# Kernel optimization log

Hardware: AMD Instinct MI355X
Metric: run time of the kernel (lower is better)

The kernel has to match this reference:

```python
import jax, jax.numpy as jnp
import numpy as np

N = 100000
E = 1600000
D_PCA = 50
D_BIO = 64
HID = 32
HEADS = 4
OUT = 50
EPS = 1e-5


def setup_inputs() -> dict:
    key = jax.random.key(0)
    ks = jax.random.split(key, 32)
    g = lambda i, shape, s=0.05: jax.random.normal(ks[i], shape, dtype=jnp.float32) * s
    inp = {
        'x_pca': jax.random.normal(ks[0], (N, D_PCA), dtype=jnp.float32),
        'x_bio': jax.random.normal(ks[1], (N, D_BIO), dtype=jnp.float32),
        'edge_index': jax.random.randint(ks[2], (2, E), 0, N, dtype=jnp.int32),
        # bio encoder: Linear(64,16) -> BN(16) -> ELU -> Linear(16,16) -> ELU
        'bioW1': g(3, (16, D_BIO)), 'biob1': g(4, (16,)),
        'bn0_g': 1.0 + g(5, (16,)), 'bn0_b': g(6, (16,)),
        'bn0_m': g(7, (16,)), 'bn0_v': 1.0 + 0.1 * jax.random.uniform(ks[8], (16,), dtype=jnp.float32),
        'bioW2': g(9, (16, 16)), 'biob2': g(10, (16,)),
        # GATv2 layer 1: in = 50+16 = 66, out = HEADS*HID concat
        'Wl1': g(11, (HEADS * HID, D_PCA + 16)), 'bl1': g(12, (HEADS * HID,)),
        'Wr1': g(13, (HEADS * HID, D_PCA + 16)), 'br1': g(14, (HEADS * HID,)),
        'att1': g(15, (HEADS, HID)), 'bias1': g(16, (HEADS * HID,)),
        'bn1_g': 1.0 + g(17, (HEADS * HID,)), 'bn1_b': g(18, (HEADS * HID,)),
        'bn1_m': g(19, (HEADS * HID,)), 'bn1_v': 1.0 + 0.1 * jax.random.uniform(ks[20], (HEADS * HID,), dtype=jnp.float32),
        # GATv2 layer 2: in = HEADS*HID, heads=1, concat=False
        'Wl2': g(21, (HID, HEADS * HID)), 'bl2': g(22, (HID,)),
        'Wr2': g(23, (HID, HEADS * HID)), 'br2': g(24, (HID,)),
        'att2': g(25, (1, HID)), 'bias2': g(26, (HID,)),
        'bn2_g': 1.0 + g(27, (HID,)), 'bn2_b': g(28, (HID,)),
        'bn2_m': g(29, (HID,)), 'bn2_v': 1.0 + 0.1 * jax.random.uniform(ks[30], (HID,), dtype=jnp.float32),
        'predW': g(31, (OUT, HID)), 'predb': jnp.zeros((OUT,), dtype=jnp.float32),
    }
    return inp


def _bn(h, gm, bt, mean, var):
    # BatchNorm1d in eval mode (running stats)
    return (h - mean) * jax.lax.rsqrt(var + EPS) * gm + bt


def _gatv2(x, src, dst, Wl, bl, Wr, br, att, bias, heads, out_dim, concat):
    n = x.shape[0]
    xl = (x @ Wl.T + bl).reshape(n, heads, out_dim)  # source transform
    xr = (x @ Wr.T + br).reshape(n, heads, out_dim)  # target transform
    e = jax.nn.leaky_relu(xl[src] + xr[dst], 0.2)    # [E,H,C]
    logits = jnp.einsum('ehc,hc->eh', e, att)        # [E,H]
    m = jax.ops.segment_max(logits, dst, num_segments=n)
    a = jnp.exp(logits - m[dst])
    denom = jax.ops.segment_sum(a, dst, num_segments=n)
    alpha = a / (denom[dst] + 1e-16)                 # segment softmax over dst
    out = jax.ops.segment_sum(xl[src] * alpha[..., None], dst, num_segments=n)
    out = out.reshape(n, heads * out_dim) if concat else out.mean(axis=1)
    return out + bias


def reference(x_pca, x_bio, edge_index,
              bioW1, biob1, bn0_g, bn0_b, bn0_m, bn0_v, bioW2, biob2,
              Wl1, bl1, Wr1, br1, att1, bias1, bn1_g, bn1_b, bn1_m, bn1_v,
              Wl2, bl2, Wr2, br2, att2, bias2, bn2_g, bn2_b, bn2_m, bn2_v,
              predW, predb):
    n = x_pca.shape[0]
    # add self-loops (PyG GATv2Conv default)
    loop = jnp.arange(n, dtype=edge_index.dtype)
    src = jnp.concatenate([edge_index[0], loop])
    dst = jnp.concatenate([edge_index[1], loop])

    # bio encoder
    h_bio = jax.nn.elu(_bn(x_bio @ bioW1.T + biob1, bn0_g, bn0_b, bn0_m, bn0_v))
    h_bio = jax.nn.elu(h_bio @ bioW2.T + biob2)
    x = jnp.concatenate([x_pca, h_bio], axis=1)  # [N, 66]

    h = _gatv2(x, src, dst, Wl1, bl1, Wr1, br1, att1, bias1, HEADS, HID, True)
    h = jax.nn.elu(_bn(h, bn1_g, bn1_b, bn1_m, bn1_v))  # dropout off (eval)
    h = _gatv2(h, src, dst, Wl2, bl2, Wr2, br2, att2, bias2, 1, HID, False)
    h = jax.nn.elu(_bn(h, bn2_g, bn2_b, bn2_m, bn2_v))
    return h @ predW.T + predb
```

## Files before the change

kernel.cpp:

```cpp
#include <hip/hip_runtime.h>
#include <hip/hip_fp16.h>
#include <cstdint>
#include <cstddef>

#define NN 100000
#define NE 1600000
#define NEP (NE + NN)
#define NBLK 200
#define CHUNK ((NEP + NBLK - 1) / NBLK)
#define NBUCK2 ((NN + 255) / 256)
#define HISTN (NBUCK2 * NBLK)
#define HSCAN_BLOCKS ((HISTN + 1023) / 1024)

typedef __attribute__((ext_vector_type(8))) _Float16 half8;
typedef __attribute__((ext_vector_type(4))) float float4v;

__device__ __forceinline__ float elu_f(float x) {
    return x > 0.f ? x : __expf(x) - 1.f;
}

template<int N>
__device__ __forceinline__ float rrot_add(float x) {
    int s = __builtin_amdgcn_update_dpp(0, __float_as_int(x), 0x120 | N, 0xF, 0xF, true);
    return x + __int_as_float(s);
}
__device__ __forceinline__ float row16_allsum(float x) {
    x = rrot_add<1>(x); x = rrot_add<2>(x); x = rrot_add<4>(x); x = rrot_add<8>(x);
    return x;
}


__global__ __launch_bounds__(256) void part_hist(const int* __restrict__ ei, int* __restrict__ hist)
{
    __shared__ int cnt[NBUCK2];
    int tid = threadIdx.x, k = blockIdx.x;
    for (int i = tid; i < NBUCK2; i += 256) cnt[i] = 0;
    __syncthreads();
    int e0 = k * CHUNK, e1 = min(e0 + CHUNK, NEP);
    for (int e = e0 + tid; e < e1; e += 256) {
        int dst = (e < NE) ? ei[NE + e] : e - NE;
        atomicAdd(&cnt[dst >> 8], 1);
    }
    __syncthreads();
    for (int i = tid; i < NBUCK2; i += 256) hist[i * NBLK + k] = cnt[i];
}

__global__ __launch_bounds__(256) void scan_p1(const int* __restrict__ src, int* __restrict__ part, int n)
{
    __shared__ int wsum[4];
    int t = threadIdx.x;
    int i0 = blockIdx.x * 1024 + t * 4;
    int s = 0;
    if (i0 + 3 < n) { int4 d = *(const int4*)(src + i0); s = d.x + d.y + d.z + d.w; }
    else { for (int k = 0; k < 4; k++) if (i0 + k < n) s += src[i0 + k]; }
    for (int d = 1; d < 64; d <<= 1) s += __shfl_xor(s, d, 64);
    if ((t & 63) == 0) wsum[t >> 6] = s;
    __syncthreads();
    if (t == 0) part[blockIdx.x] = wsum[0] + wsum[1] + wsum[2] + wsum[3];
}

__global__ __launch_bounds__(128) void scan_p2(int* __restrict__ part, int nb, int* __restrict__ off)
{
    __shared__ int wt[2];
    int t = threadIdx.x;
    int lane = t & 63, w = t >> 6;
    int v = (t < nb) ? part[t] : 0;
    int x = v;
    for (int d = 1; d < 64; d <<= 1) { int y = __shfl_up(x, d, 64); if (lane >= d) x += y; }
    if (lane == 63) wt[w] = x;
    __syncthreads();
    int base = (w == 1) ? wt[0] : 0;
    int excl = base + x - v;
    if (t < nb) part[t] = excl;
    if (t == 0) off[NN] = NEP;
}

__global__ __launch_bounds__(256) void scan_p3(int* __restrict__ data, const int* __restrict__ part, int n)
{
    __shared__ int wsum[4];
    int t = threadIdx.x, lane = t & 63, w = t >> 6;
    int i0 = blockIdx.x * 1024 + t * 4;
    int d0 = 0, d1 = 0, d2 = 0, d3 = 0;
    if (i0 + 3 < n) { int4 d = *(const int4*)(data + i0); d0 = d.x; d1 = d.y; d2 = d.z; d3 = d.w; }
    else if (i0 < n) {
        d0 = data[i0];
        if (i0 + 1 < n) d1 = data[i0 + 1];
        if (i0 + 2 < n) d2 = data[i0 + 2];
    }
    int s = d0 + d1 + d2 + d3;
    int x = s;
    for (int d = 1; d < 64; d <<= 1) { int y = __shfl_up(x, d, 64); if (lane >= d) x += y; }
    if (lane == 63) wsum[w] = x;
    __syncthreads();
    int wb = 0;
    for (int i = 0; i < w; i++) wb += wsum[i];
    int base = part[blockIdx.x] + wb + x - s;
    if (i0 < n)     data[i0]     = base;
    if (i0 + 1 < n) data[i0 + 1] = base + d0;
    if (i0 + 2 < n) data[i0 + 2] = base + d0 + d1;
    if (i0 + 3 < n) data[i0 + 3] = base + d0 + d1 + d2;
}

__global__ __launch_bounds__(256) void part_scatter(const int* __restrict__ ei,
                                                    const int* __restrict__ hist,
                                                    unsigned* __restrict__ ebuf)
{
    __shared__ int cur[NBUCK2];
    int tid = threadIdx.x, k = blockIdx.x;
    for (int i = tid; i < NBUCK2; i += 256) cur[i] = hist[i * NBLK + k];
    __syncthreads();
    int e0 = k * CHUNK, e1 = min(e0 + CHUNK, NEP);
    for (int e = e0 + tid; e < e1; e += 256) {
        int src, dst;
        if (e < NE) { src = ei[e]; dst = ei[NE + e]; } else { src = dst = e - NE; }
        int pos = atomicAdd(&cur[dst >> 8], 1);
        ebuf[pos] = (unsigned)src | ((unsigned)(dst & 255) << 24);
    }
}

__global__ __launch_bounds__(256) void bucket_csr(const int* __restrict__ hist,
                                                  const unsigned* __restrict__ ebuf,
                                                  int* __restrict__ off, int* __restrict__ csr)
{
    __shared__ int cnt[256];
    __shared__ int cur[256];
    __shared__ int wsum[4];
    int b = blockIdx.x;
    int d0 = b << 8;
    int tid = threadIdx.x;
    int e0 = hist[b * NBLK];
    int e1 = (b + 1 < NBUCK2) ? hist[(b + 1) * NBLK] : NEP;
    cnt[tid] = 0;
    __syncthreads();
    for (int i = e0 + tid; i < e1; i += 256) atomicAdd(&cnt[ebuf[i] >> 24], 1);
    __syncthreads();
    int c = cnt[tid];
    int x = c;
    int lane = tid & 63, w = tid >> 6;
    for (int d = 1; d < 64; d <<= 1) { int y = __shfl_up(x, d, 64); if (lane >= d) x += y; }
    if (lane == 63) wsum[w] = x;
    __syncthreads();
    int wb = 0;
    for (int i = 0; i < w; i++) wb += wsum[i];
    int excl = wb + x - c;
    cur[tid] = e0 + excl;
    int node = d0 + tid;
    if (node < NN) off[node] = e0 + excl;
    __syncthreads();
    for (int i = e0 + tid; i < e1; i += 256) {
        unsigned v = ebuf[i];
        int p = atomicAdd(&cur[v >> 24], 1);
        csr[p] = (int)(v & 0xFFFFFF);
    }
}


__global__ __launch_bounds__(256) void bio_kernel(
    const float* __restrict__ xb, const float* __restrict__ W1, const float* __restrict__ b1,
    const float* __restrict__ g0, const float* __restrict__ bb0,
    const float* __restrict__ m0, const float* __restrict__ v0,
    const float* __restrict__ W2, const float* __restrict__ b2,
    __half* __restrict__ xh)
{
    __shared__ float sW1[16*64], sW2[16*16], sb1[16], sb2[16], ss[16], st[16];
    int tid = threadIdx.x;
    for (int idx = tid; idx < 1024; idx += 256) sW1[idx] = W1[idx];
    if (tid < 256) sW2[tid] = W2[tid];
    if (tid < 16) {
        sb1[tid] = b1[tid]; sb2[tid] = b2[tid];
        float s = g0[tid] * rsqrtf(v0[tid] + 1e-5f);
        ss[tid] = s; st[tid] = bb0[tid] - m0[tid] * s;
    }
    __syncthreads();
    int i = blockIdx.x * 256 + tid;
    if (i >= NN) return;
    float bio[64];
    const float4* p = (const float4*)(xb + (size_t)i * 64);
    #pragma unroll
    for (int q = 0; q < 16; q++) {
        float4 f = p[q];
        bio[q*4] = f.x; bio[q*4+1] = f.y; bio[q*4+2] = f.z; bio[q*4+3] = f.w;
    }
    float t1[16];
    #pragma unroll
    for (int j = 0; j < 16; j++) {
        float acc = sb1[j];
        #pragma unroll
        for (int k = 0; k < 64; k++) acc += bio[k] * sW1[j*64 + k];
        acc = acc * ss[j] + st[j];
        t1[j] = elu_f(acc);
    }
    __half* xo = xh + (size_t)i * 96 + 50;
    #pragma unroll
    for (int j = 0; j < 16; j++) {
        float acc = sb2[j];
        #pragma unroll
        for (int k = 0; k < 16; k++) acc += t1[k] * sW2[j*16 + k];
        xo[j] = __float2half(elu_f(acc));
    }
    __half2 z2 = __floats2half2_rn(0.f, 0.f);
    __half2* pz = (__half2*)(xh + (size_t)i * 96 + 66);
    #pragma unroll
    for (int j = 0; j < 15; j++) pz[j] = z2;
}

__global__ __launch_bounds__(256) void copy_pca(const float* __restrict__ xp, __half* __restrict__ xh)
{
    int t = blockIdx.x * 256 + threadIdx.x;
    if (t >= NN * 50) return;
    int i = t / 50, j = t - i * 50;
    xh[(size_t)i * 96 + j] = __float2half(xp[t]);
}


__global__ __launch_bounds__(256) void wconvert(
    const float* __restrict__ Wl, const float* __restrict__ Wr,
    const float* __restrict__ bl, const float* __restrict__ br,
    __half* __restrict__ wcat, float* __restrict__ bcat,
    int NH, int K, int KPAD)
{
    int total = 2 * NH * KPAD;
    for (int t = blockIdx.x * 256 + threadIdx.x; t < total; t += gridDim.x * 256) {
        int j = t / KPAD, k = t - j * KPAD;
        float v = 0.f;
        if (k < K) v = (j < NH) ? Wl[j * K + k] : Wr[(j - NH) * K + k];
        wcat[t] = __float2half(v);
    }
    int t = blockIdx.x * 256 + threadIdx.x;
    if (t < 2 * NH) bcat[t] = (t < NH) ? bl[t] : br[t - NH];
}

__global__ __launch_bounds__(256) void wpred_conv(
    const float* __restrict__ W, const float* __restrict__ bias,
    __half* __restrict__ wp, float* __restrict__ bp)
{
    int t = blockIdx.x * 256 + threadIdx.x;
    if (t < 64 * 32) {
        int j = t >> 5;
        wp[t] = __float2half(j < 50 ? W[t - ((j - 50 >= 0) ? 0 : 0)] : 0.f);
        if (j < 50) wp[t] = __float2half(W[t]); else wp[t] = __float2half(0.f);
    }
    if (t < 64) bp[t] = (t < 50) ? bias[t] : 0.f;
}

template<int KT, int NC, bool FOUT>
__global__ __launch_bounds__(256) void mfma_gemm(
    const __half* __restrict__ in, const __half* __restrict__ wcat,
    const float* __restrict__ bcat, void* __restrict__ outv, int n, int ncol)
{
    constexpr int K = KT * 32;
    constexpr int KP = K + 8;
    __shared__ __half sW[NC * KP];
    __shared__ __half sX[64 * KP];
    __shared__ float sB[NC];
    int tid = threadIdx.x;
    for (int idx = tid * 8; idx < NC * K; idx += 256 * 8) {
        int r = idx / K, c = idx - r * K;
        *(half8*)(&sW[r * KP + c]) = *(const half8*)(&wcat[r * K + c]);
    }
    for (int idx = tid; idx < NC; idx += 256) sB[idx] = bcat[idx];
    int row0 = blockIdx.x * 64;
    half8 hz = {0, 0, 0, 0, 0, 0, 0, 0};
    for (int idx = tid * 8; idx < 64 * K; idx += 256 * 8) {
        int r = idx / K, c = idx - r * K;
        int gr = row0 + r;
        half8 v = (gr < n) ? *(const half8*)(&in[(size_t)gr * K + c]) : hz;
        *(half8*)(&sX[r * KP + c]) = v;
    }
    __syncthreads();
    int w = tid >> 6, lane = tid & 63;
    int m = lane & 15, quad = lane >> 4;
    half8 a[KT];
    #pragma unroll
    for (int kt = 0; kt < KT; kt++)
        a[kt] = *(const half8*)(&sX[(w * 16 + m) * KP + kt * 32 + quad * 8]);
    #pragma unroll 1
    for (int nt = 0; nt < NC / 16; nt++) {
        float4v acc = {0.f, 0.f, 0.f, 0.f};
        #pragma unroll
        for (int kt = 0; kt < KT; kt++) {
            half8 bfrag = *(const half8*)(&sW[(nt * 16 + m) * KP + kt * 32 + quad * 8]);
            acc = __builtin_amdgcn_mfma_f32_16x16x32_f16(a[kt], bfrag, acc, 0, 0, 0);
        }
        int col = nt * 16 + m;
        float bias = sB[col];
        #pragma unroll
        for (int i = 0; i < 4; i++) {
            int r = row0 + w * 16 + quad * 4 + i;
            if (r < n) {
                if (FOUT) { if (col < ncol) ((float*)outv)[(size_t)r * ncol + col] = acc[i] + bias; }
                else ((__half*)outv)[(size_t)r * NC + col] = __float2half(acc[i] + bias);
            }
        }
    }
}

__global__ __launch_bounds__(256) void fused_gat1(
    const int* __restrict__ off, const int* __restrict__ csr,
    const __half2* __restrict__ xcat, const float* __restrict__ att,
    const float* __restrict__ bias, const float* __restrict__ g,
    const float* __restrict__ b, const float* __restrict__ m,
    const float* __restrict__ v, __half2* __restrict__ h1)
{
    int wave = threadIdx.x >> 6;
    int lane = threadIdx.x & 63;
    int node = blockIdx.x * 4 + wave;
    if (node >= NN) return;
    int ch = lane * 2;

    float2 xrv = __half22float2(xcat[(size_t)node * 128 + 64 + lane]);
    float2 av  = *(const float2*)(att + ch);

    int k0 = off[node], k1 = off[node + 1];
    float accx = 0.f, accy = 0.f, denom = 0.f;

    for (int base = k0; base < k1; base += 64) {
        int nb = min(64, k1 - base);
        int mysrc = (lane < nb) ? csr[base + lane] : 0;
        int cs = __builtin_amdgcn_readlane(mysrc, 0);
        __half2 hcur = xcat[(size_t)cs * 128 + lane];
        for (int t = 0; t < nb; t++) {
            int tn = (t + 1 < nb) ? t + 1 : t;
            int ns = __builtin_amdgcn_readlane(mysrc, tn);
            __half2 hnxt = xcat[(size_t)ns * 128 + lane];
            float2 xlv = __half22float2(hcur);
            float sx = xlv.x + xrv.x; sx = fmaxf(sx, 0.2f * sx);
            float sy = xlv.y + xrv.y; sy = fmaxf(sy, 0.2f * sy);
            float pp = sx * av.x + sy * av.y;
            pp = row16_allsum(pp);
            float wgt = __expf(pp);
            denom += wgt;
            accx = fmaf(xlv.x, wgt, accx);
            accy = fmaf(xlv.y, wgt, accy);
            hcur = hnxt;
        }
    }
    float inv = 1.f / (denom + 1e-16f);
    float sX = g[ch]     * rsqrtf(v[ch]     + 1e-5f);
    float sY = g[ch + 1] * rsqrtf(v[ch + 1] + 1e-5f);
    float ox = accx * inv + bias[ch];
    float oy = accy * inv + bias[ch + 1];
    ox = ox * sX + (b[ch]     - m[ch]     * sX);
    oy = oy * sY + (b[ch + 1] - m[ch + 1] * sY);
    h1[(size_t)node * 64 + lane] = __floats2half2_rn(elu_f(ox), elu_f(oy));
}

__global__ __launch_bounds__(256) void fused_gat2(
    const int* __restrict__ off, const int* __restrict__ csr,
    const __half2* __restrict__ xcat2, const float* __restrict__ att,
    const float* __restrict__ bias, const float* __restrict__ g,
    const float* __restrict__ b, const float* __restrict__ m,
    const float* __restrict__ v, __half2* __restrict__ h2)
{
    int wave = threadIdx.x >> 6;
    int lane = threadIdx.x & 63;
    int node = blockIdx.x * 4 + wave;
    if (node >= NN) return;
    int row = lane >> 4;
    int cp  = lane & 15;
    int c   = cp * 2;

    float2 xrv = __half22float2(xcat2[(size_t)node * 32 + 16 + cp]);
    float2 av  = *(const float2*)(att + c);

    int k0 = off[node], k1 = off[node + 1];
    float accx = 0.f, accy = 0.f, denom = 0.f;

    for (int base = k0; base < k1; base += 64) {
        int nb = min(64, k1 - base);
        int mysrc = (lane < nb) ? csr[base + lane] : 0;
        for (int t = 0; t < nb; t += 4) {
            int i1 = min(t + 1, nb - 1), i2 = min(t + 2, nb - 1), i3 = min(t + 3, nb - 1);
            int s0 = __builtin_amdgcn_readlane(mysrc, t);
            int s1 = __builtin_amdgcn_readlane(mysrc, i1);
            int s2 = __builtin_amdgcn_readlane(mysrc, i2);
            int s3 = __builtin_amdgcn_readlane(mysrc, i3);
            int sa  = (row & 1) ? s1 : s0;
            int sb_ = (row & 1) ? s3 : s2;
            int ss  = (row & 2) ? sb_ : sa;
            float2 xlv = __half22float2(xcat2[(size_t)ss * 32 + cp]);
            float sx = xlv.x + xrv.x; sx = fmaxf(sx, 0.2f * sx);
            float sy = xlv.y + xrv.y; sy = fmaxf(sy, 0.2f * sy);
            float pp = sx * av.x + sy * av.y;
            pp = row16_allsum(pp);
            bool valid = (t + row) < nb;
            float wgt = valid ? __expf(pp) : 0.f;
            denom += wgt;
            accx = fmaf(xlv.x, wgt, accx);
            accy = fmaf(xlv.y, wgt, accy);
        }
    }
    accx  += __shfl_xor(accx, 16, 64);  accx  += __shfl_xor(accx, 32, 64);
    accy  += __shfl_xor(accy, 16, 64);  accy  += __shfl_xor(accy, 32, 64);
    denom += __shfl_xor(denom, 16, 64); denom += __shfl_xor(denom, 32, 64);
    if (row == 0) {
        float inv = 1.f / (denom + 1e-16f);
        float sC0 = g[c]     * rsqrtf(v[c]     + 1e-5f);
        float sC1 = g[c + 1] * rsqrtf(v[c + 1] + 1e-5f);
        float o0 = accx * inv + bias[c];
        float o1 = accy * inv + bias[c + 1];
        o0 = o0 * sC0 + (b[c]     - m[c]     * sC0);
        o1 = o1 * sC1 + (b[c + 1] - m[c + 1] * sC1);
        h2[(size_t)node * 16 + cp] = __floats2half2_rn(elu_f(o0), elu_f(o1));
    }
}

extern "C" void kernel_launch(void* const* d_in, const int* in_sizes, int n_in,
                              void* d_out, int out_size, void* d_ws, size_t ws_size,
                              hipStream_t stream)
{
    const float* x_pca = (const float*)d_in[0];
    const float* x_bio = (const float*)d_in[1];
    const int*   ei    = (const int*)d_in[2];
    const float* bioW1 = (const float*)d_in[3];
    const float* biob1 = (const float*)d_in[4];
    const float* bn0_g = (const float*)d_in[5];
    const float* bn0_b = (const float*)d_in[6];
    const float* bn0_m = (const float*)d_in[7];
    const float* bn0_v = (const float*)d_in[8];
    const float* bioW2 = (const float*)d_in[9];
    const float* biob2 = (const float*)d_in[10];
    const float* Wl1   = (const float*)d_in[11];
    const float* bl1   = (const float*)d_in[12];
    const float* Wr1   = (const float*)d_in[13];
    const float* br1   = (const float*)d_in[14];
    const float* att1  = (const float*)d_in[15];
    const float* bias1 = (const float*)d_in[16];
    const float* bn1_g = (const float*)d_in[17];
    const float* bn1_b = (const float*)d_in[18];
    const float* bn1_m = (const float*)d_in[19];
    const float* bn1_v = (const float*)d_in[20];
    const float* Wl2   = (const float*)d_in[21];
    const float* bl2   = (const float*)d_in[22];
    const float* Wr2   = (const float*)d_in[23];
    const float* br2   = (const float*)d_in[24];
    const float* att2  = (const float*)d_in[25];
    const float* bias2 = (const float*)d_in[26];
    const float* bn2_g = (const float*)d_in[27];
    const float* bn2_b = (const float*)d_in[28];
    const float* bn2_m = (const float*)d_in[29];
    const float* bn2_v = (const float*)d_in[30];
    const float* predW = (const float*)d_in[31];
    const float* predb = (const float*)d_in[32];

    float* ws = (float*)d_ws;
    __half* xh    = (__half*)ws;
    float*  p0    = ws + 4800000;
    __half* xcat1 = (__half*)p0;
    float*  p1    = p0 + 12800000;
    __half* h1h   = (__half*)p1;
    float*  p2    = p1 + 6400000;
    __half* xcat2 = (__half*)p2;
    float*  p3    = p2 + 3200000;
    __half* h2h   = (__half*)p3;
    float*  p4    = p3 + 1600000;
    __half* wcat1 = (__half*)p4;
    float*  bcat1 = p4 + 12288;
    __half* wcat2 = (__half*)(bcat1 + 256);
    float*  bcat2 = bcat1 + 256 + 4096;
    __half* wpred = (__half*)(bcat2 + 64);
    float*  bpred = bcat2 + 64 + 1024;
    int*    ib    = (int*)(bpred + 64);
    unsigned* ebuf = (unsigned*)ib;
    int*    hist   = ib + NEP;
    int*    part   = hist + HISTN;
    int*    off    = part + 128;
    int*    csr    = off + NN + 1;

    float* out = (float*)d_out;

    part_hist<<<NBLK, 256, 0, stream>>>(ei, hist);
    scan_p1<<<HSCAN_BLOCKS, 256, 0, stream>>>(hist, part, HISTN);
    scan_p2<<<1, 128, 0, stream>>>(part, HSCAN_BLOCKS, off);
    scan_p3<<<HSCAN_BLOCKS, 256, 0, stream>>>(hist, part, HISTN);
    part_scatter<<<NBLK, 256, 0, stream>>>(ei, hist, ebuf);
    bucket_csr<<<NBUCK2, 256, 0, stream>>>(hist, ebuf, off, csr);

    bio_kernel<<<(NN + 255) / 256, 256, 0, stream>>>(
        x_bio, bioW1, biob1, bn0_g, bn0_b, bn0_m, bn0_v, bioW2, biob2, xh);
    copy_pca<<<(NN * 50 + 255) / 256, 256, 0, stream>>>(x_pca, xh);

    wconvert<<<96, 256, 0, stream>>>(Wl1, Wr1, bl1, br1, wcat1, bcat1, 128, 66, 96);
    wconvert<<<32, 256, 0, stream>>>(Wl2, Wr2, bl2, br2, wcat2, bcat2, 32, 128, 128);
    wpred_conv<<<8, 256, 0, stream>>>(predW, predb, wpred, bpred);

    mfma_gemm<3, 256, false><<<(NN + 63) / 64, 256, 0, stream>>>(xh, wcat1, bcat1, xcat1, NN, 0);

    fused_gat1<<<(NN + 3) / 4, 256, 0, stream>>>(
        off, csr, (const __half2*)xcat1, att1, bias1, bn1_g, bn1_b, bn1_m, bn1_v, (__half2*)h1h);

    mfma_gemm<4, 64, false><<<(NN + 63) / 64, 256, 0, stream>>>(h1h, wcat2, bcat2, xcat2, NN, 0);

    fused_gat2<<<(NN + 3) / 4, 256, 0, stream>>>(
        off, csr, (const __half2*)xcat2, att2, bias2, bn2_g, bn2_b, bn2_m, bn2_v, (__half2*)h2h);

    mfma_gemm<1, 64, true><<<(NN + 63) / 64, 256, 0, stream>>>(h2h, wpred, bpred, out, NN, 50);
}
```

Measured before the change: 481.8 us.

## Pack two edges per wave in GAT1, use fp16 dot2, fuse prep kernels

```diff
diff --git a/kernel.cpp b/kernel.cpp
--- a/kernel.cpp
+++ b/kernel.cpp
@@ -13,20 +13,43 @@
 #define HSCAN_BLOCKS ((HISTN + 1023) / 1024)
 
 typedef __attribute__((ext_vector_type(8))) _Float16 half8;
+typedef __attribute__((ext_vector_type(4))) _Float16 h4v;
+typedef __attribute__((ext_vector_type(2))) _Float16 h2v;
 typedef __attribute__((ext_vector_type(4))) float float4v;
 
 __device__ __forceinline__ float elu_f(float x) {
     return x > 0.f ? x : __expf(x) - 1.f;
 }
 
-template<int N>
-__device__ __forceinline__ float rrot_add(float x) {
-    int s = __builtin_amdgcn_update_dpp(0, __float_as_int(x), 0x120 | N, 0xF, 0xF, true);
+template<int CTRL>
+__device__ __forceinline__ float dpp_add(float x) {
+    int s = __builtin_amdgcn_update_dpp(0, __float_as_int(x), CTRL, 0xF, 0xF, true);
     return x + __int_as_float(s);
 }
-__device__ __forceinline__ float row16_allsum(float x) {
-    x = rrot_add<1>(x); x = rrot_add<2>(x); x = rrot_add<4>(x); x = rrot_add<8>(x);
+__device__ __forceinline__ float sum8_all(float x) {
+    x = dpp_add<0xB1>(x); x = dpp_add<0x4E>(x); x = dpp_add<0x141>(x);
     return x;
+}
+__device__ __forceinline__ float sum16_all(float x) {
+    x = dpp_add<0xB1>(x); x = dpp_add<0x4E>(x); x = dpp_add<0x141>(x); x = dpp_add<0x140>(x);
+    return x;
+}
+
+__device__ __forceinline__ float dot2f(h2v a, h2v b, float c) {
+#if __has_builtin(__builtin_amdgcn_fdot2)
+    return __builtin_amdgcn_fdot2(a, b, c, false);
+#else
+    return fmaf((float)a[0], (float)b[0], fmaf((float)a[1], (float)b[1], c));
+#endif
+}
+
+__device__ __forceinline__ h2v hmax2v(h2v a, h2v b) {
+#if __has_builtin(__builtin_elementwise_max)
+    return __builtin_elementwise_max(a, b);
+#else
+    __half2 r = __hmax2(*(__half2*)&a, *(__half2*)&b);
+    return *(h2v*)&r;
+#endif
 }
 
 
@@ -156,7 +179,8 @@
 
 
 __global__ __launch_bounds__(256) void bio_kernel(
-    const float* __restrict__ xb, const float* __restrict__ W1, const float* __restrict__ b1,
+    const float* __restrict__ xb, const float* __restrict__ xp,
+    const float* __restrict__ W1, const float* __restrict__ b1,
     const float* __restrict__ g0, const float* __restrict__ bb0,
     const float* __restrict__ m0, const float* __restrict__ v0,
     const float* __restrict__ W2, const float* __restrict__ b2,
@@ -190,57 +214,59 @@
         acc = acc * ss[j] + st[j];
         t1[j] = elu_f(acc);
     }
-    __half* xo = xh + (size_t)i * 96 + 50;
+    __half* xrow = xh + (size_t)i * 96;
+    const float* xpr = xp + (size_t)i * 50;
+    #pragma unroll
+    for (int j = 0; j < 25; j++) {
+        float2 f = *(const float2*)(xpr + 2 * j);
+        *(__half2*)(xrow + 2 * j) = __floats2half2_rn(f.x, f.y);
+    }
     #pragma unroll
     for (int j = 0; j < 16; j++) {
         float acc = sb2[j];
         #pragma unroll
         for (int k = 0; k < 16; k++) acc += t1[k] * sW2[j*16 + k];
-        xo[j] = __float2half(elu_f(acc));
+        xrow[50 + j] = __float2half(elu_f(acc));
     }
     __half2 z2 = __floats2half2_rn(0.f, 0.f);
-    __half2* pz = (__half2*)(xh + (size_t)i * 96 + 66);
     #pragma unroll
-    for (int j = 0; j < 15; j++) pz[j] = z2;
-}
-
-__global__ __launch_bounds__(256) void copy_pca(const float* __restrict__ xp, __half* __restrict__ xh)
+    for (int j = 0; j < 15; j++) *(__half2*)(xrow + 66 + 2 * j) = z2;
+}
+
+
+__global__ __launch_bounds__(256) void wconvert_all(
+    const float* __restrict__ Wl1, const float* __restrict__ Wr1,
+    const float* __restrict__ bl1, const float* __restrict__ br1,
+    const float* __restrict__ Wl2, const float* __restrict__ Wr2,
+    const float* __restrict__ bl2, const float* __restrict__ br2,
+    const float* __restrict__ predW, const float* __restrict__ predb,
+    __half* __restrict__ wcat1, float* __restrict__ bcat1,
+    __half* __restrict__ wcat2, float* __restrict__ bcat2,
+    __half* __restrict__ wpred, float* __restrict__ bpred)
 {
     int t = blockIdx.x * 256 + threadIdx.x;
-    if (t >= NN * 50) return;
-    int i = t / 50, j = t - i * 50;
-    xh[(size_t)i * 96 + j] = __float2half(xp[t]);
-}
-
-
-__global__ __launch_bounds__(256) void wconvert(
-    const float* __restrict__ Wl, const float* __restrict__ Wr,
-    const float* __restrict__ bl, const float* __restrict__ br,
-    __half* __restrict__ wcat, float* __restrict__ bcat,
-    int NH, int K, int KPAD)
-{
-    int total = 2 * NH * KPAD;
-    for (int t = blockIdx.x * 256 + threadIdx.x; t < total; t += gridDim.x * 256) {
-        int j = t / KPAD, k = t - j * KPAD;
-        float v = 0.f;
-        if (k < K) v = (j < NH) ? Wl[j * K + k] : Wr[(j - NH) * K + k];
-        wcat[t] = __float2half(v);
-    }
-    int t = blockIdx.x * 256 + threadIdx.x;
-    if (t < 2 * NH) bcat[t] = (t < NH) ? bl[t] : br[t - NH];
-}
-
-__global__ __launch_bounds__(256) void wpred_conv(
-    const float* __restrict__ W, const float* __restrict__ bias,
-    __half* __restrict__ wp, float* __restrict__ bp)
-{
-    int t = blockIdx.x * 256 + threadIdx.x;
-    if (t < 64 * 32) {
-        int j = t >> 5;
-        wp[t] = __float2half(j < 50 ? W[t - ((j - 50 >= 0) ? 0 : 0)] : 0.f);
-        if (j < 50) wp[t] = __float2half(W[t]); else wp[t] = __float2half(0.f);
-    }
-    if (t < 64) bp[t] = (t < 50) ? bias[t] : 0.f;
+    if (t < 256 * 96) {
+        int j = t / 96, k = t - j * 96;
+        float v = (k < 66) ? ((j < 128) ? Wl1[j * 66 + k] : Wr1[(j - 128) * 66 + k]) : 0.f;
+        wcat1[t] = __float2half(v);
+    }
+    int u = t - 256 * 96;
+    if (u >= 0 && u < 64 * 128) {
+        int j = u >> 7, k = u & 127;
+        float v = (j < 32) ? Wl2[j * 128 + k] : Wr2[(j - 32) * 128 + k];
+        wcat2[u] = __float2half(v);
+    }
+    int w = u - 64 * 128;
+    if (w >= 0 && w < 64 * 32) {
+        int j = w >> 5;
+        wpred[w] = __float2half(j < 50 ? predW[w] : 0.f);
+    }
+    int z = w - 64 * 32;
+    if (z >= 0 && z < 256) bcat1[z] = (z < 128) ? bl1[z] : br1[z - 128];
+    int z2 = z - 256;
+    if (z2 >= 0 && z2 < 64) bcat2[z2] = (z2 < 32) ? bl2[z2] : br2[z2 - 32];
+    int z3 = z2 - 64;
+    if (z3 >= 0 && z3 < 64) bpred[z3] = (z3 < 50) ? predb[z3] : 0.f;
 }
 
 template<int KT, int NC, bool FOUT>
@@ -297,60 +323,91 @@
 
 __global__ __launch_bounds__(256) void fused_gat1(
     const int* __restrict__ off, const int* __restrict__ csr,
-    const __half2* __restrict__ xcat, const float* __restrict__ att,
+    const __half* __restrict__ xcat, const float* __restrict__ att,
     const float* __restrict__ bias, const float* __restrict__ g,
     const float* __restrict__ b, const float* __restrict__ m,
-    const float* __restrict__ v, __half2* __restrict__ h1)
+    const float* __restrict__ v, __half* __restrict__ h1)
 {
     int wave = threadIdx.x >> 6;
     int lane = threadIdx.x & 63;
     int node = blockIdx.x * 4 + wave;
     if (node >= NN) return;
-    int ch = lane * 2;
-
-    float2 xrv = __half22float2(xcat[(size_t)node * 128 + 64 + lane]);
-    float2 av  = *(const float2*)(att + ch);
+    int slot = lane >> 5;
+    int l = lane & 31;
+    int ch = l * 4;
+
+    h4v xr4 = *(const h4v*)(xcat + (size_t)node * 256 + 128 + ch);
+    h2v xr01 = {xr4[0], xr4[1]}, xr23 = {xr4[2], xr4[3]};
+    float4 af = *(const float4*)(att + ch);
+    h2v a01 = {(_Float16)af.x, (_Float16)af.y};
+    h2v a23 = {(_Float16)af.z, (_Float16)af.w};
+    const h2v c2 = {(_Float16)0.2f, (_Float16)0.2f};
 
     int k0 = off[node], k1 = off[node + 1];
-    float accx = 0.f, accy = 0.f, denom = 0.f;
+    float acc0 = 0.f, acc1 = 0.f, acc2 = 0.f, acc3 = 0.f, denom = 0.f;
 
     for (int base = k0; base < k1; base += 64) {
         int nb = min(64, k1 - base);
         int mysrc = (lane < nb) ? csr[base + lane] : 0;
-        int cs = __builtin_amdgcn_readlane(mysrc, 0);
-        __half2 hcur = xcat[(size_t)cs * 128 + lane];
-        for (int t = 0; t < nb; t++) {
-            int tn = (t + 1 < nb) ? t + 1 : t;
-            int ns = __builtin_amdgcn_readlane(mysrc, tn);
-            __half2 hnxt = xcat[(size_t)ns * 128 + lane];
-            float2 xlv = __half22float2(hcur);
-            float sx = xlv.x + xrv.x; sx = fmaxf(sx, 0.2f * sx);
-            float sy = xlv.y + xrv.y; sy = fmaxf(sy, 0.2f * sy);
-            float pp = sx * av.x + sy * av.y;
-            pp = row16_allsum(pp);
-            float wgt = __expf(pp);
+        int p0 = __builtin_amdgcn_readlane(mysrc, 0);
+        int p1 = __builtin_amdgcn_readlane(mysrc, nb > 1 ? 1 : 0);
+        int ssel = slot ? p1 : p0;
+        h4v cur = *(const h4v*)(xcat + (size_t)(unsigned)ssel * 256 + ch);
+        for (int t = 0; t < nb; t += 2) {
+            int t2 = (t + 2 < nb) ? t + 2 : nb - 1;
+            int t3 = (t + 3 < nb) ? t + 3 : nb - 1;
+            int n0 = __builtin_amdgcn_readlane(mysrc, t2);
+            int n1 = __builtin_amdgcn_readlane(mysrc, t3);
+            int nsel = slot ? n1 : n0;
+            h4v nxt = *(const h4v*)(xcat + (size_t)(unsigned)nsel * 256 + ch);
+
+            h2v xl01 = {cur[0], cur[1]}, xl23 = {cur[2], cur[3]};
+            h2v s01 = xl01 + xr01, s23 = xl23 + xr23;
+            h2v ls01 = hmax2v(s01, s01 * c2);
+            h2v ls23 = hmax2v(s23, s23 * c2);
+            float pp = dot2f(ls01, a01, dot2f(ls23, a23, 0.f));
+            pp = sum8_all(pp);
+            bool valid = (t + slot) < nb;
+            float wgt = valid ? __expf(pp) : 0.f;
             denom += wgt;
-            accx = fmaf(xlv.x, wgt, accx);
-            accy = fmaf(xlv.y, wgt, accy);
-            hcur = hnxt;
+            acc0 = fmaf((float)cur[0], wgt, acc0);
+            acc1 = fmaf((float)cur[1], wgt, acc1);
+            acc2 = fmaf((float)cur[2], wgt, acc2);
+            acc3 = fmaf((float)cur[3], wgt, acc3);
+            cur = nxt;
         }
     }
-    float inv = 1.f / (denom + 1e-16f);
-    float sX = g[ch]     * rsqrtf(v[ch]     + 1e-5f);
-    float sY = g[ch + 1] * rsqrtf(v[ch + 1] + 1e-5f);
-    float ox = accx * inv + bias[ch];
-    float oy = accy * inv + bias[ch + 1];
-    ox = ox * sX + (b[ch]     - m[ch]     * sX);
-    oy = oy * sY + (b[ch + 1] - m[ch + 1] * sY);
-    h1[(size_t)node * 64 + lane] = __floats2half2_rn(elu_f(ox), elu_f(oy));
+    acc0 += __shfl_xor(acc0, 32, 64);
+    acc1 += __shfl_xor(acc1, 32, 64);
+    acc2 += __shfl_xor(acc2, 32, 64);
+    acc3 += __shfl_xor(acc3, 32, 64);
+    denom += __shfl_xor(denom, 32, 64);
+    if (slot == 0) {
+        float inv = 1.f / (denom + 1e-16f);
+        float4 gv = *(const float4*)(g + ch);
+        float4 vv = *(const float4*)(v + ch);
+        float4 bv = *(const float4*)(b + ch);
+        float4 mv = *(const float4*)(m + ch);
+        float4 biv = *(const float4*)(bias + ch);
+        float s0 = gv.x * rsqrtf(vv.x + 1e-5f);
+        float s1 = gv.y * rsqrtf(vv.y + 1e-5f);
+        float s2 = gv.z * rsqrtf(vv.z + 1e-5f);
+        float s3 = gv.w * rsqrtf(vv.w + 1e-5f);
+        float o0 = elu_f((acc0 * inv + biv.x) * s0 + (bv.x - mv.x * s0));
+        float o1 = elu_f((acc1 * inv + biv.y) * s1 + (bv.y - mv.y * s1));
+        float o2 = elu_f((acc2 * inv + biv.z) * s2 + (bv.z - mv.z * s2));
+        float o3 = elu_f((acc3 * inv + biv.w) * s3 + (bv.w - mv.w * s3));
+        h4v o = {(_Float16)o0, (_Float16)o1, (_Float16)o2, (_Float16)o3};
+        *(h4v*)(h1 + (size_t)node * 128 + ch) = o;
+    }
 }
 
 __global__ __launch_bounds__(256) void fused_gat2(
     const int* __restrict__ off, const int* __restrict__ csr,
-    const __half2* __restrict__ xcat2, const float* __restrict__ att,
+    const __half* __restrict__ xcat2, const float* __restrict__ att,
     const float* __restrict__ bias, const float* __restrict__ g,
     const float* __restrict__ b, const float* __restrict__ m,
-    const float* __restrict__ v, __half2* __restrict__ h2)
+    const float* __restrict__ v, __half* __restrict__ h2)
 {
     int wave = threadIdx.x >> 6;
     int lane = threadIdx.x & 63;
@@ -360,8 +417,10 @@
     int cp  = lane & 15;
     int c   = cp * 2;
 
-    float2 xrv = __half22float2(xcat2[(size_t)node * 32 + 16 + cp]);
-    float2 av  = *(const float2*)(att + c);
+    h2v xr = *(const h2v*)(xcat2 + (size_t)node * 64 + 32 + c);
+    float2 af = *(const float2*)(att + c);
+    h2v ah = {(_Float16)af.x, (_Float16)af.y};
+    const h2v c2 = {(_Float16)0.2f, (_Float16)0.2f};
 
     int k0 = off[node], k1 = off[node + 1];
     float accx = 0.f, accy = 0.f, denom = 0.f;
@@ -378,16 +437,16 @@
             int sa  = (row & 1) ? s1 : s0;
             int sb_ = (row & 1) ? s3 : s2;
             int ss  = (row & 2) ? sb_ : sa;
-            float2 xlv = __half22float2(xcat2[(size_t)ss * 32 + cp]);
-            float sx = xlv.x + xrv.x; sx = fmaxf(sx, 0.2f * sx);
-            float sy = xlv.y + xrv.y; sy = fmaxf(sy, 0.2f * sy);
-            float pp = sx * av.x + sy * av.y;
-            pp = row16_allsum(pp);
+            h2v xl = *(const h2v*)(xcat2 + (size_t)(unsigned)ss * 64 + c);
+            h2v s = xl + xr;
+            h2v ls = hmax2v(s, s * c2);
+            float pp = dot2f(ls, ah, 0.f);
+            pp = sum16_all(pp);
             bool valid = (t + row) < nb;
             float wgt = valid ? __expf(pp) : 0.f;
             denom += wgt;
-            accx = fmaf(xlv.x, wgt, accx);
-            accy = fmaf(xlv.y, wgt, accy);
+            accx = fmaf((float)xl[0], wgt, accx);
+            accy = fmaf((float)xl[1], wgt, accy);
         }
     }
     accx  += __shfl_xor(accx, 16, 64);  accx  += __shfl_xor(accx, 32, 64);
@@ -397,11 +456,9 @@
         float inv = 1.f / (denom + 1e-16f);
         float sC0 = g[c]     * rsqrtf(v[c]     + 1e-5f);
         float sC1 = g[c + 1] * rsqrtf(v[c + 1] + 1e-5f);
-        float o0 = accx * inv + bias[c];
-        float o1 = accy * inv + bias[c + 1];
-        o0 = o0 * sC0 + (b[c]     - m[c]     * sC0);
-        o1 = o1 * sC1 + (b[c + 1] - m[c + 1] * sC1);
-        h2[(size_t)node * 16 + cp] = __floats2half2_rn(elu_f(o0), elu_f(o1));
+        float o0 = elu_f((accx * inv + bias[c])     * sC0 + (b[c]     - m[c]     * sC0));
+        float o1 = elu_f((accy * inv + bias[c + 1]) * sC1 + (b[c + 1] - m[c + 1] * sC1));
+        *(__half2*)(h2 + (size_t)node * 32 + c) = __floats2half2_rn(o0, o1);
     }
 }
 
@@ -477,22 +534,21 @@
     bucket_csr<<<NBUCK2, 256, 0, stream>>>(hist, ebuf, off, csr);
 
     bio_kernel<<<(NN + 255) / 256, 256, 0, stream>>>(
-        x_bio, bioW1, biob1, bn0_g, bn0_b, bn0_m, bn0_v, bioW2, biob2, xh);
-    copy_pca<<<(NN * 50 + 255) / 256, 256, 0, stream>>>(x_pca, xh);
-
-    wconvert<<<96, 256, 0, stream>>>(Wl1, Wr1, bl1, br1, wcat1, bcat1, 128, 66, 96);
-    wconvert<<<32, 256, 0, stream>>>(Wl2, Wr2, bl2, br2, wcat2, bcat2, 32, 128, 128);
-    wpred_conv<<<8, 256, 0, stream>>>(predW, predb, wpred, bpred);
+        x_bio, x_pca, bioW1, biob1, bn0_g, bn0_b, bn0_m, bn0_v, bioW2, biob2, xh);
+
+    wconvert_all<<<138, 256, 0, stream>>>(
+        Wl1, Wr1, bl1, br1, Wl2, Wr2, bl2, br2, predW, predb,
+        wcat1, bcat1, wcat2, bcat2, wpred, bpred);
 
     mfma_gemm<3, 256, false><<<(NN + 63) / 64, 256, 0, stream>>>(xh, wcat1, bcat1, xcat1, NN, 0);
 
     fused_gat1<<<(NN + 3) / 4, 256, 0, stream>>>(
-        off, csr, (const __half2*)xcat1, att1, bias1, bn1_g, bn1_b, bn1_m, bn1_v, (__half2*)h1h);
+        off, csr, xcat1, att1, bias1, bn1_g, bn1_b, bn1_m, bn1_v, h1h);
 
     mfma_gemm<4, 64, false><<<(NN + 63) / 64, 256, 0, stream>>>(h1h, wcat2, bcat2, xcat2, NN, 0);
 
     fused_gat2<<<(NN + 3) / 4, 256, 0, stream>>>(
-        off, csr, (const __half2*)xcat2, att2, bias2, bn2_g, bn2_b, bn2_m, bn2_v, (__half2*)h2h);
+        off, csr, xcat2, att2, bias2, bn2_g, bn2_b, bn2_m, bn2_v, h2h);
 
     mfma_gemm<1, 64, true><<<(NN + 63) / 64, 256, 0, stream>>>(h2h, wpred, bpred, out, NN, 50);
 }
```

Result: faster. 432.3 us (-10.3%).
